# Performance work log

Hardware: AMD Instinct MI355X
Metric: run time of the kernel (lower is better)

## Reference

```python
import jax, jax.numpy as jnp
import numpy as np

N = 50000      # nodes
E = 800000     # edges (avg degree 16)
H = 128        # hidden_dim
F_IN = 128     # node_in_dim
EPS = 1e-8     # torch cosine_similarity eps
ALPHA = 0.3


def _xavier(k, shape):
    fan_out, fan_in = shape
    lim = float(np.sqrt(6.0 / (fan_in + fan_out)))
    return jax.random.uniform(k, shape, minval=-lim, maxval=lim, dtype=jnp.float32)


PARAM_SHAPES = [
    ("w_lq", (H, 1)), ("w_lf", (H, F_IN)),
    ("wq0", (H, 1)), ("wq1", (H, H)), ("wq2", (H, H)),
    ("wx0", (H, F_IN)), ("wx1", (H, H)), ("wx2", (H, H)),
    ("wf0", (H, H)), ("wf1", (H, H)), ("wf2", (H, H)),
    ("m1_w1", (H, H)), ("m1_w2", (H, H)),
    ("m2_w1", (1, H)), ("m2_w2", (1, 1)),
]
BIAS_OF = {"w_lq": "b_lq", "w_lf": "b_lf", "wq0": "bq0", "wq1": "bq1", "wq2": "bq2",
           "wx0": "bx0", "wx1": "bx1", "wx2": "bx2", "wf0": "bf0", "wf1": "bf1",
           "wf2": "bf2", "m1_w1": "m1_b1", "m1_w2": "m1_b2", "m2_w1": "m2_b1", "m2_w2": "m2_b2"}


def setup_inputs() -> dict:
    key = jax.random.key(0)
    ks = jax.random.split(key, 3 + len(PARAM_SHAPES))
    inp = {
        "q": 42,
        "feats": jax.random.normal(ks[0], (N, F_IN), dtype=jnp.float32),
        "edge_index": jax.random.randint(ks[1], (2, E), 0, N, dtype=jnp.int64),
        "neg_edge_index": jax.random.randint(ks[2], (2, E), 0, N, dtype=jnp.int64),
    }
    for i, (name, shape) in enumerate(PARAM_SHAPES):
        inp[name] = _xavier(ks[3 + i], shape)
        inp[BIAS_OF[name]] = jnp.zeros((shape[0],), jnp.float32)
    return inp


def _forward(q, feats, edge_index, neg_edge_index,
             w_lq, b_lq, w_lf, b_lf,
             wq0, bq0, wq1, bq1, wq2, bq2,
             wx0, bx0, wx1, bx1, wx2, bx2,
             wf0, bf0, wf1, bf1, wf2, bf2,
             m1_w1, m1_b1, m1_w2, m1_b2,
             m2_w1, m2_b1, m2_w2, m2_b2):
    n = feats.shape[0]
    src, dst = edge_index[0], edge_index[1]

    # GCN symmetric normalization with self-loops (edge_weight = 1)
    deg = jax.ops.segment_sum(jnp.ones(src.shape[0], feats.dtype), dst, num_segments=n) + 1.0
    dis = deg ** -0.5
    norm_e = dis[src] * dis[dst]        # per-edge norm
    inv_deg = 1.0 / deg                 # self-loop norm d^-1/2 * d^-1/2

    def lin(x, W, b):
        return x @ W.T + b

    def gcn(x, W, b):
        xw = x @ W.T                                                      # [n,H]
        agg = jax.ops.segment_sum(xw[src] * norm_e[:, None], dst, num_segments=n)
        return agg + xw * inv_deg[:, None] + b

    querys = jnp.zeros((n, 1), feats.dtype).at[q, 0].set(1.0)
    querys_ = lin(querys, w_lq, b_lq)
    feats_ = lin(feats, w_lf, b_lf)

    # layer 0
    hq = jax.nn.relu(gcn(querys, wq0, bq0))
    h = jax.nn.relu(gcn(feats, wx0, bx0))
    hf = jax.nn.relu(hq + h + gcn(querys_ + feats_, wf0, bf0))
    # middle layer (num_layers - 2 == 1 iteration, eval mode: dropout identity)
    hq = jax.nn.relu(gcn(hq, wq1, bq1))
    h = jax.nn.relu(gcn(h, wx1, bx1))
    hf = jax.nn.relu(hq + h + gcn(hf, wf1, bf1))
    # final layer (no relu)
    hq = gcn(hq, wq2, bq2)
    h = gcn(h, wx2, bx2)
    hf = hq + h + gcn(hf, wf2, bf2)

    x = lin(jax.nn.relu(lin(hf, m1_w1, m1_b1)), m1_w2, m1_b2)  # mlp1

    # ---- decode (attack_type != 'proposed') ----
    q_emb = x[q]
    qn = jnp.maximum(jnp.linalg.norm(q_emb), EPS)

    def cos_q(v):  # cosine similarity of rows of v with q_emb (torch eps semantics)
        vn = jnp.maximum(jnp.linalg.norm(v, axis=-1), EPS)
        return (v @ q_emb) / (vn * qn)

    # reconstruct loss: BCE-with-logits on cosine edge scores
    pos_s = cos_q((x[src] + x[dst]) * 0.5)
    neg_s = cos_q((x[neg_edge_index[0]] + x[neg_edge_index[1]]) * 0.5)
    loss_recon = jnp.mean(jax.nn.softplus(-pos_s)) + jnp.mean(jax.nn.softplus(neg_s))

    sim_xq = cos_q(x)                                            # [n]
    sim_xx = lin(jax.nn.relu(lin(x, m2_w1, m2_b1)), m2_w2, m2_b2)[:, 0]  # mlp2
    sim = ((1.0 - ALPHA) * sim_xq + ALPHA * sim_xx) * 2.0
    return jax.nn.sigmoid(sim), loss_recon


def reference(q, feats, edge_index, neg_edge_index,
              w_lq, b_lq, w_lf, b_lf,
              wq0, bq0, wq1, bq1, wq2, bq2,
              wx0, bx0, wx1, bx1, wx2, bx2,
              wf0, bf0, wf1, bf1, wf2, bf2,
              m1_w1, m1_b1, m1_w2, m1_b2,
              m2_w1, m2_b1, m2_w2, m2_b2):
    return _forward(q, feats, edge_index, neg_edge_index,
                    w_lq, b_lq, w_lf, b_lf,
                    wq0, bq0, wq1, bq1, wq2, bq2,
                    wx0, bx0, wx1, bx1, wx2, bx2,
                    wf0, bf0, wf1, bf1, wf2, bf2,
                    m1_w1, m1_b1, m1_w2, m1_b2,
                    m2_w1, m2_b1, m2_w2, m2_b2)
```

## Files before the change

### kernel.cpp

```cpp
#include <hip/hip_runtime.h>
#include <math.h>

#define N_NODES 50000
#define N_EDGES 800000
#define EPSV 1e-8f
#define ALPHA 0.3f

typedef __attribute__((ext_vector_type(8))) unsigned short ushort8;
typedef __attribute__((ext_vector_type(8))) short short8;
typedef __attribute__((ext_vector_type(4))) float floatx4;
typedef _Float16 half2v __attribute__((ext_vector_type(2)));

__device__ inline float b2f(unsigned short u) {
    union { unsigned i; float f; } c; c.i = ((unsigned)u) << 16; return c.f;
}
__device__ inline unsigned short f2b(float f) {
    union { float f; unsigned i; } c; c.f = f;
    return (unsigned short)((c.i + 0x7FFFu + ((c.i >> 16) & 1u)) >> 16);
}
__device__ inline unsigned short f2h(float f) {
    union { _Float16 h; unsigned short u; } c; c.h = (_Float16)f; return c.u;
}


__global__ __launch_bounds__(256) void k_count(const int* __restrict__ ei,
                                               int* __restrict__ cnt) {
    int e = blockIdx.x * 256 + threadIdx.x;
    if (e < N_EDGES) atomicAdd(&cnt[ei[N_EDGES + e]], 1);
}

__global__ __launch_bounds__(256) void k_invdis(const int* __restrict__ cnt,
                                                float* __restrict__ dis,
                                                float* __restrict__ inv) {
    int i = blockIdx.x * 256 + threadIdx.x;
    if (i < N_NODES) {
        float d = (float)cnt[i] + 1.0f;
        dis[i] = 1.0f / sqrtf(d);
        inv[i] = 1.0f / d;
    }
}

__global__ __launch_bounds__(256) void k_scan_partial(const int* __restrict__ cnt,
                                                      int* __restrict__ partial) {
    int b = blockIdx.x, t = threadIdx.x;
    int base = b * 1024 + t * 4;
    int s = 0;
#pragma unroll
    for (int j = 0; j < 4; ++j) {
        int idx = base + j;
        if (idx < N_NODES) s += cnt[idx];
    }
#pragma unroll
    for (int m = 1; m < 64; m <<= 1) s += __shfl_xor(s, m, 64);
    __shared__ int sh[4];
    if ((t & 63) == 0) sh[t >> 6] = s;
    __syncthreads();
    if (t == 0) partial[b] = sh[0] + sh[1] + sh[2] + sh[3];
}

__global__ void k_scan_mid(int* __restrict__ partial, int* __restrict__ rowptr) {
    int l = threadIdx.x;
    const int NP = (N_NODES + 1023) / 1024;
    int v = (l < NP) ? partial[l] : 0;
    int vin = v;
#pragma unroll
    for (int off = 1; off < 64; off <<= 1) {
        int u = __shfl_up(v, off, 64);
        if (l >= off) v += u;
    }
    if (l < NP) partial[l] = v - vin;
    if (l == NP - 1) rowptr[N_NODES] = v;
}

__global__ __launch_bounds__(256) void k_scan_final(const int* __restrict__ cnt,
                                                    const int* __restrict__ partial,
                                                    int* __restrict__ rowptr) {
    int b = blockIdx.x, t = threadIdx.x;
    int base = b * 1024 + t * 4;
    int c[4];
    int s = 0;
#pragma unroll
    for (int j = 0; j < 4; ++j) {
        int idx = base + j;
        c[j] = (idx < N_NODES) ? cnt[idx] : 0;
        s += c[j];
    }
    __shared__ int sh[256];
    sh[t] = s;
    __syncthreads();
    for (int off = 1; off < 256; off <<= 1) {
        int v = 0;
        if (t >= off) v = sh[t - off];
        __syncthreads();
        sh[t] += v;
        __syncthreads();
    }
    int texcl = sh[t] - s;
    int pre = partial[b] + texcl;
#pragma unroll
    for (int j = 0; j < 4; ++j) {
        int idx = base + j;
        if (idx < N_NODES) rowptr[idx] = pre;
        pre += c[j];
    }
}

__global__ __launch_bounds__(256) void k_fill(const int* __restrict__ ei,
                                              const int* __restrict__ rowptr,
                                              int* __restrict__ cursor,
                                              int* __restrict__ col) {
    int e = blockIdx.x * 256 + threadIdx.x;
    if (e < N_EDGES) {
        int d = ei[N_EDGES + e];
        int pos = rowptr[d] + atomicAdd(&cursor[d], 1);
        col[pos] = ei[e];
    }
}

__global__ __launch_bounds__(256) void k_t(const int* __restrict__ ei,
                                           const int* __restrict__ qp,
                                           const float* __restrict__ dis,
                                           const float* __restrict__ inv,
                                           float* __restrict__ t) {
    int e = blockIdx.x * 256 + threadIdx.x;
    int q = *qp;
    if (e == 0) atomicAdd(&t[q], inv[q]);
    if (e < N_EDGES && ei[e] == q) {
        int d = ei[N_EDGES + e];
        atomicAdd(&t[d], dis[q] * dis[d]);
    }
}

__global__ __launch_bounds__(256) void k_cast(const float* __restrict__ in,
                                              unsigned short* __restrict__ out, int n8) {
    int id = blockIdx.x * 256 + threadIdx.x;
    if (id >= n8) return;
    const float4 a = *(const float4*)(in + id * 8);
    const float4 b = *(const float4*)(in + id * 8 + 4);
    ushort8 o;
    o[0] = f2b(a.x); o[1] = f2b(a.y); o[2] = f2b(a.z); o[3] = f2b(a.w);
    o[4] = f2b(b.x); o[5] = f2b(b.y); o[6] = f2b(b.z); o[7] = f2b(b.w);
    *(ushort8*)(out + id * 8) = o;
}

struct WPack { const float* w[11]; };
__global__ __launch_bounds__(256) void k_castw(WPack wp, unsigned short* __restrict__ out) {
    int m = blockIdx.y;
    int id = blockIdx.x * 256 + threadIdx.x;
    const float* src = wp.w[m] + id * 8;
    float4 a = *(const float4*)src;
    float4 b = *(const float4*)(src + 4);
    ushort8 o;
    o[0] = f2b(a.x); o[1] = f2b(a.y); o[2] = f2b(a.z); o[3] = f2b(a.w);
    o[4] = f2b(b.x); o[5] = f2b(b.y); o[6] = f2b(b.z); o[7] = f2b(b.w);
    *(ushort8*)(out + m * 16384 + id * 8) = o;
}


template <int RELU, int NADD, int HASB2, int WOUT>
__global__ __launch_bounds__(256) void k_gemm(
    const unsigned short* __restrict__ A, int As,
    const unsigned short* __restrict__ Wb,
    const float* __restrict__ bias, const float* __restrict__ bias2,
    const unsigned short* __restrict__ add1, int a1s,
    const unsigned short* __restrict__ add2, int a2s,
    unsigned short* __restrict__ outh, int ohs,
    float* __restrict__ outf, int ofs, int nrows) {
    __shared__ unsigned short Al[128 * 128];
    __shared__ unsigned short Wl[128 * 128];
    const int tid = threadIdx.x;
    const int row0 = blockIdx.x * 128;
    const int wv = tid >> 6;
    const int t4 = tid >> 4, c16 = tid & 15;

#pragma unroll
    for (int it = 0; it < 8; ++it) {
        int r = it * 16 + t4;
        int gr = row0 + r; if (gr > nrows - 1) gr = nrows - 1;
        int sw = (c16 * 16) ^ ((r & 7) << 4);
        const char* srcA = (const char*)(A + (size_t)gr * As) + sw;
        __builtin_amdgcn_global_load_lds(
            (const __attribute__((address_space(1))) void*)srcA,
            (__attribute__((address_space(3))) void*)(Al + it * 2048 + wv * 512),
            16, 0, 0);
        const char* srcW = (const char*)(Wb + r * 128) + sw;
        __builtin_amdgcn_global_load_lds(
            (const __attribute__((address_space(1))) void*)srcW,
            (__attribute__((address_space(3))) void*)(Wl + it * 2048 + wv * 512),
            16, 0, 0);
    }
    __syncthreads();

    const int l = tid & 63;
    const int lr = l & 15, lg = l >> 4;
    const int sx = (lr & 7) << 4;

    floatx4 acc[8][2];
#pragma unroll
    for (int i = 0; i < 8; ++i)
#pragma unroll
        for (int j = 0; j < 2; ++j) acc[i][j] = (floatx4){0.f, 0.f, 0.f, 0.f};

#pragma unroll
    for (int ks = 0; ks < 4; ++ks) {
        int ko = (ks * 64 + lg * 16) ^ sx;
        short8 bfr[2];
#pragma unroll
        for (int ct = 0; ct < 2; ++ct) {
            int c = wv * 32 + ct * 16 + lr;
            bfr[ct] = *(const short8*)((char*)Wl + c * 256 + ko);
        }
#pragma unroll
        for (int rt = 0; rt < 8; ++rt) {
            int r = rt * 16 + lr;
            short8 af = *(const short8*)((char*)Al + r * 256 + ko);
            acc[rt][0] = __builtin_amdgcn_mfma_f32_16x16x32_bf16(af, bfr[0], acc[rt][0], 0, 0, 0);
            acc[rt][1] = __builtin_amdgcn_mfma_f32_16x16x32_bf16(af, bfr[1], acc[rt][1], 0, 0, 0);
        }
    }

#pragma unroll
    for (int ct = 0; ct < 2; ++ct) {
        int colc = wv * 32 + ct * 16 + lr;
        float bv = bias[colc];
        if (HASB2) bv += bias2[colc];
#pragma unroll
        for (int rt = 0; rt < 8; ++rt) {
            int rbase = row0 + rt * 16 + lg * 4;
#pragma unroll
            for (int reg = 0; reg < 4; ++reg) {
                int r = rbase + reg;
                if (r >= nrows) continue;
                float v = acc[rt][ct][reg] + bv;
                if (NADD >= 1) v += b2f(add1[(size_t)r * a1s + colc]);
                if (NADD >= 2) v += b2f(add2[(size_t)r * a2s + colc]);
                if (RELU) v = fmaxf(v, 0.f);
                if (WOUT) {
                    outh[(size_t)r * ohs + colc] = f2h(v);
                    outf[(size_t)r * ofs + colc] = v;
                } else {
                    outh[(size_t)r * ohs + colc] = f2b(v);
                }
            }
        }
    }
}


__global__ __launch_bounds__(256) void k_agg(
    const int* __restrict__ rowptr, const int* __restrict__ col,
    const float* __restrict__ dis, const float* __restrict__ inv,
    const unsigned short* __restrict__ in, int ins,
    unsigned short* __restrict__ out, int outs, int outcb) {
    int i = blockIdx.x * 4 + (threadIdx.x >> 6);
    int cb = blockIdx.y * 128;
    int l = threadIdx.x & 63;
    int g = l >> 4, li = l & 15;
    int r0 = rowptr[i], r1 = rowptr[i + 1];
    float acc[8] = {0.f, 0.f, 0.f, 0.f, 0.f, 0.f, 0.f, 0.f};
    for (int base = r0; base < r1; base += 4) {
        int e = base + g;
        float w = 0.f;
        int s = i;
        if (e < r1) { s = col[e]; w = dis[s]; }
        ushort8 v = *(const ushort8*)(in + (size_t)s * ins + cb + li * 8);
#pragma unroll
        for (int j = 0; j < 8; ++j) acc[j] = fmaf(w, b2f(v[j]), acc[j]);
    }
#pragma unroll
    for (int j = 0; j < 8; ++j) {
        acc[j] += __shfl_xor(acc[j], 16, 64);
        acc[j] += __shfl_xor(acc[j], 32, 64);
    }
    if (g == 0) {
        ushort8 sv = *(const ushort8*)(in + (size_t)i * ins + cb + li * 8);
        float di = dis[i], iv = inv[i];
        ushort8 o;
#pragma unroll
        for (int j = 0; j < 8; ++j) o[j] = f2b(fmaf(di, acc[j], iv * b2f(sv[j])));
        *(ushort8*)(out + (size_t)i * outs + outcb + cb + li * 8) = o;
    }
}

__global__ __launch_bounds__(256) void k_hq0(const float* __restrict__ t,
                                             const float* __restrict__ wq0,
                                             const float* __restrict__ bq0,
                                             unsigned short* __restrict__ B1h) {
    int gidx = blockIdx.x * 256 + threadIdx.x;
    int i = gidx >> 7, j = gidx & 127;
    B1h[(size_t)i * 384 + j] = f2b(fmaxf(fmaf(t[i], wq0[j], bq0[j]), 0.f));
}

__global__ void k_addwlq(const int* __restrict__ qp, const float* __restrict__ w_lq,
                         unsigned short* __restrict__ z0h) {
    int j = threadIdx.x;
    int q = *qp;
    z0h[(size_t)q * 128 + j] = f2b(b2f(z0h[(size_t)q * 128 + j]) + w_lq[j]);
}


__global__ void k_qemb(const int* __restrict__ qp, const float* __restrict__ xf,
                       float* __restrict__ qe) {
    int j = threadIdx.x;
    int q = *qp;
    float v = xf[(size_t)q * 128 + j];
    qe[j] = v;
    float s = v * v;
#pragma unroll
    for (int m = 1; m < 64; m <<= 1) s += __shfl_xor(s, m, 64);
    __shared__ float sh[2];
    if ((j & 63) == 0) sh[j >> 6] = s;
    __syncthreads();
    if (j == 0) qe[128] = fmaxf(sqrtf(sh[0] + sh[1]), EPSV);
}

__global__ __launch_bounds__(256) void k_node(const float* __restrict__ xf,
                                              const float* __restrict__ qe,
                                              const float* __restrict__ m2w1,
                                              const float* __restrict__ m2b1,
                                              const float* __restrict__ m2w2,
                                              const float* __restrict__ m2b2,
                                              float* __restrict__ out,
                                              float* __restrict__ a,
                                              float* __restrict__ n2) {
    int node = blockIdx.x * 4 + (threadIdx.x >> 6);
    int lane = threadIdx.x & 63;
    const float2 xv = *(const float2*)(xf + (size_t)node * 128 + 2 * lane);
    const float2 qv = *(const float2*)(qe + 2 * lane);
    const float2 wv = *(const float2*)(m2w1 + 2 * lane);
    float dq = xv.x * qv.x + xv.y * qv.y;
    float dx = xv.x * xv.x + xv.y * xv.y;
    float dw = xv.x * wv.x + xv.y * wv.y;
#pragma unroll
    for (int m = 1; m < 64; m <<= 1) {
        dq += __shfl_xor(dq, m, 64);
        dx += __shfl_xor(dx, m, 64);
        dw += __shfl_xor(dw, m, 64);
    }
    if (lane == 0) {
        float qn = qe[128];
        float vn = fmaxf(sqrtf(dx), EPSV);
        float simq = dq / (vn * qn);
        float l1 = dw + m2b1[0];
        float s2 = fmaxf(l1, 0.f) * m2w2[0] + m2b2[0];
        float sim = ((1.f - ALPHA) * simq + ALPHA * s2) * 2.f;
        out[node] = 1.f / (1.f + expf(-sim));
        a[node] = dq;
        n2[node] = dx;
    }
}

__global__ __launch_bounds__(256) void k_loss(const int* __restrict__ ei,
                                              const int* __restrict__ nei,
                                              const unsigned short* __restrict__ xh,
                                              const float* __restrict__ a,
                                              const float* __restrict__ n2,
                                              const float* __restrict__ qe,
                                              float* __restrict__ lossout) {
    int l = threadIdx.x & 63, wvi = threadIdx.x >> 6;
    int g = l >> 4, li = l & 15;
    float qn = qe[128];
    float local = 0.f;
    const int tot = 2 * N_EDGES;
    const int stride = gridDim.x * 16;
    for (int e = blockIdx.x * 16 + wvi * 4 + g; e < tot; e += stride) {
        const int* Ep = (e < N_EDGES) ? ei : nei;
        int eo = (e < N_EDGES) ? e : e - N_EDGES;
        int s = Ep[eo], d = Ep[eo + N_EDGES];
        union { ushort8 u; half2v h[4]; } va, vb;
        va.u = *(const ushort8*)(xh + (size_t)s * 128 + li * 8);
        vb.u = *(const ushort8*)(xh + (size_t)d * 128 + li * 8);
        float dsd = 0.f;
#pragma unroll
        for (int j = 0; j < 4; ++j)
            dsd = __builtin_amdgcn_fdot2(va.h[j], vb.h[j], dsd, false);
        dsd += __shfl_xor(dsd, 1, 64);
        dsd += __shfl_xor(dsd, 2, 64);
        dsd += __shfl_xor(dsd, 4, 64);
        dsd += __shfl_xor(dsd, 8, 64);
        if (li == 0) {
            float nv = 0.25f * (n2[s] + n2[d] + 2.f * dsd);
            float vn = fmaxf(sqrtf(fmaxf(nv, 0.f)), EPSV);
            float num = 0.5f * (a[s] + a[d]);
            float cs = num / (vn * qn);
            float sg = (e < N_EDGES) ? -cs : cs;
            local += log1pf(expf(sg));
        }
    }
    local += __shfl_xor(local, 16, 64);
    local += __shfl_xor(local, 32, 64);
    __shared__ float sh[4];
    if (l == 0) sh[wvi] = local;
    __syncthreads();
    if (threadIdx.x == 0)
        atomicAdd(lossout, (sh[0] + sh[1] + sh[2] + sh[3]) * (1.f / N_EDGES));
}


extern "C" void kernel_launch(void* const* d_in, const int* in_sizes, int n_in,
                              void* d_out, int out_size, void* d_ws, size_t ws_size,
                              hipStream_t stream) {
    const int* qp = (const int*)d_in[0];
    const float* feats = (const float*)d_in[1];
    const int* ei = (const int*)d_in[2];
    const int* nei = (const int*)d_in[3];
    const float *w_lq = (const float*)d_in[4], *b_lq = (const float*)d_in[5];
    const float *w_lf = (const float*)d_in[6], *b_lf = (const float*)d_in[7];
    const float *wq0 = (const float*)d_in[8], *bq0 = (const float*)d_in[9];
    const float *wq1 = (const float*)d_in[10], *bq1 = (const float*)d_in[11];
    const float *wq2 = (const float*)d_in[12], *bq2 = (const float*)d_in[13];
    const float *wx0 = (const float*)d_in[14], *bx0 = (const float*)d_in[15];
    const float *wx1 = (const float*)d_in[16], *bx1 = (const float*)d_in[17];
    const float *wx2 = (const float*)d_in[18], *bx2 = (const float*)d_in[19];
    const float *wf0 = (const float*)d_in[20], *bf0 = (const float*)d_in[21];
    const float *wf1 = (const float*)d_in[22], *bf1 = (const float*)d_in[23];
    const float *wf2 = (const float*)d_in[24], *bf2 = (const float*)d_in[25];
    const float *m1w1 = (const float*)d_in[26], *m1b1 = (const float*)d_in[27];
    const float *m1w2 = (const float*)d_in[28], *m1b2 = (const float*)d_in[29];
    const float *m2w1 = (const float*)d_in[30], *m2b1 = (const float*)d_in[31];
    const float *m2w2 = (const float*)d_in[32], *m2b2 = (const float*)d_in[33];
    float* out = (float*)d_out;

    char* p = (char*)d_ws;
    auto alloc = [&](size_t b) -> char* {
        char* r = p;
        p += (b + 255) & ~(size_t)255;
        return r;
    };
    float* dis = (float*)alloc(N_NODES * 4);
    float* inv = (float*)alloc(N_NODES * 4);
    float* t = (float*)alloc(N_NODES * 4);
    float* qe = (float*)alloc(129 * 4);
    float* a = (float*)alloc(N_NODES * 4);
    float* n2 = (float*)alloc(N_NODES * 4);
    int* cnt = (int*)alloc(N_NODES * 4);
    int* cursor = (int*)alloc(N_NODES * 4);
    int* rowptr = (int*)alloc((N_NODES + 1) * 4);
    int* partial = (int*)alloc(64 * 4);
    int* col = (int*)alloc(N_EDGES * 4);
    unsigned short* Wb = (unsigned short*)alloc((size_t)11 * 16384 * 2);
    unsigned short* featsh = (unsigned short*)alloc((size_t)N_NODES * 128 * 2);
    unsigned short* z0h = (unsigned short*)alloc((size_t)N_NODES * 128 * 2);
    unsigned short* B1h = (unsigned short*)alloc((size_t)N_NODES * 384 * 2);
    unsigned short* B2h = (unsigned short*)alloc((size_t)N_NODES * 384 * 2);
    unsigned short* xh = (unsigned short*)alloc((size_t)N_NODES * 128 * 2);
    float* xf = (float*)alloc((size_t)N_NODES * 128 * 4);

    const int EB = (N_EDGES + 255) / 256;
    const int NB = (N_NODES + 255) / 256;
    const int NP = (N_NODES + 1023) / 1024;
    const int GB = (N_NODES + 127) / 128;

    hipMemsetAsync(cnt, 0, N_NODES * 4, stream);
    hipMemsetAsync(cursor, 0, N_NODES * 4, stream);
    hipMemsetAsync(t, 0, N_NODES * 4, stream);
    hipMemsetAsync(out + N_NODES, 0, 4, stream);

    k_count<<<EB, 256, 0, stream>>>(ei, cnt);
    k_invdis<<<NB, 256, 0, stream>>>(cnt, dis, inv);
    k_scan_partial<<<NP, 256, 0, stream>>>(cnt, partial);
    k_scan_mid<<<1, 64, 0, stream>>>(partial, rowptr);
    k_scan_final<<<NP, 256, 0, stream>>>(cnt, partial, rowptr);
    k_fill<<<EB, 256, 0, stream>>>(ei, rowptr, cursor, col);
    k_t<<<EB, 256, 0, stream>>>(ei, qp, dis, inv, t);
    k_cast<<<(N_NODES * 128 / 8 + 255) / 256, 256, 0, stream>>>(feats, featsh,
                                                                N_NODES * 128 / 8);
    WPack wp{{w_lf, wx0, wf0, wq1, wx1, wf1, wq2, wx2, wf2, m1w1, m1w2}};
    k_castw<<<dim3(8, 11), 256, 0, stream>>>(wp, Wb);

    k_gemm<0, 0, 1, 0><<<GB, 256, 0, stream>>>(featsh, 128, Wb + 0 * 16384, b_lf, b_lq,
                                               nullptr, 0, nullptr, 0,
                                               z0h, 128, nullptr, 0, N_NODES);
    k_addwlq<<<1, 128, 0, stream>>>(qp, w_lq, z0h);

    k_hq0<<<(N_NODES * 128) / 256, 256, 0, stream>>>(t, wq0, bq0, B1h);
    k_agg<<<dim3(N_NODES / 4, 1), 256, 0, stream>>>(rowptr, col, dis, inv, featsh, 128,
                                                    B2h, 384, 128);
    k_agg<<<dim3(N_NODES / 4, 1), 256, 0, stream>>>(rowptr, col, dis, inv, z0h, 128,
                                                    B2h, 384, 256);
    k_gemm<1, 0, 0, 0><<<GB, 256, 0, stream>>>(B2h + 128, 384, Wb + 1 * 16384, bx0, nullptr,
                                               nullptr, 0, nullptr, 0,
                                               B1h + 128, 384, nullptr, 0, N_NODES);
    k_gemm<1, 2, 0, 0><<<GB, 256, 0, stream>>>(B2h + 256, 384, Wb + 2 * 16384, bf0, nullptr,
                                               B1h + 0, 384, B1h + 128, 384,
                                               B1h + 256, 384, nullptr, 0, N_NODES);

    k_agg<<<dim3(N_NODES / 4, 3), 256, 0, stream>>>(rowptr, col, dis, inv, B1h, 384,
                                                    B2h, 384, 0);
    k_gemm<1, 0, 0, 0><<<GB, 256, 0, stream>>>(B2h + 0, 384, Wb + 3 * 16384, bq1, nullptr,
                                               nullptr, 0, nullptr, 0,
                                               B1h + 0, 384, nullptr, 0, N_NODES);
    k_gemm<1, 0, 0, 0><<<GB, 256, 0, stream>>>(B2h + 128, 384, Wb + 4 * 16384, bx1, nullptr,
                                               nullptr, 0, nullptr, 0,
                                               B1h + 128, 384, nullptr, 0, N_NODES);
    k_gemm<1, 2, 0, 0><<<GB, 256, 0, stream>>>(B2h + 256, 384, Wb + 5 * 16384, bf1, nullptr,
                                               B1h + 0, 384, B1h + 128, 384,
                                               B1h + 256, 384, nullptr, 0, N_NODES);

    k_agg<<<dim3(N_NODES / 4, 3), 256, 0, stream>>>(rowptr, col, dis, inv, B1h, 384,
                                                    B2h, 384, 0);
    k_gemm<0, 0, 0, 0><<<GB, 256, 0, stream>>>(B2h + 0, 384, Wb + 6 * 16384, bq2, nullptr,
                                               nullptr, 0, nullptr, 0,
                                               B1h + 0, 384, nullptr, 0, N_NODES);
    k_gemm<0, 0, 0, 0><<<GB, 256, 0, stream>>>(B2h + 128, 384, Wb + 7 * 16384, bx2, nullptr,
                                               nullptr, 0, nullptr, 0,
                                               B1h + 128, 384, nullptr, 0, N_NODES);
    k_gemm<0, 2, 0, 0><<<GB, 256, 0, stream>>>(B2h + 256, 384, Wb + 8 * 16384, bf2, nullptr,
                                               B1h + 0, 384, B1h + 128, 384,
                                               B1h + 256, 384, nullptr, 0, N_NODES);

    k_gemm<1, 0, 0, 0><<<GB, 256, 0, stream>>>(B1h + 256, 384, Wb + 9 * 16384, m1b1, nullptr,
                                               nullptr, 0, nullptr, 0,
                                               B2h + 0, 384, nullptr, 0, N_NODES);
    k_gemm<0, 0, 0, 1><<<GB, 256, 0, stream>>>(B2h + 0, 384, Wb + 10 * 16384, m1b2, nullptr,
                                               nullptr, 0, nullptr, 0,
                                               xh, 128, xf, 128, N_NODES);

    k_qemb<<<1, 128, 0, stream>>>(qp, xf, qe);
    k_node<<<N_NODES / 4, 256, 0, stream>>>(xf, qe, m2w1, m2b1, m2w2, m2b2, out, a, n2);
    k_loss<<<4096, 256, 0, stream>>>(ei, nei, xh, a, n2, qe, out + N_NODES);
}
```

Measured before the change: 737.4 us.

## Switch intermediates to fp16, fuse multi-branch aggregation, use MFMA for edge dots

All intermediate activations and weights move from bf16 to fp16, and the GEMMs now use the f16 MFMA. The aggregation kernel handles two or three feature branches per launch and accumulates with packed half2 FMAs instead of fp32. The loss kernel computes the edge dot products with 16x16 MFMA tiles plus a bpermute instead of fdot2 and shuffle reductions. Accumulating in fp16 halves ALU and register cost but risks precision loss or overflow on high-degree nodes.

```diff
diff --git a/kernel.cpp b/kernel.cpp
--- a/kernel.cpp
+++ b/kernel.cpp
@@ -7,19 +7,15 @@
 #define ALPHA 0.3f
 
 typedef __attribute__((ext_vector_type(8))) unsigned short ushort8;
-typedef __attribute__((ext_vector_type(8))) short short8;
 typedef __attribute__((ext_vector_type(4))) float floatx4;
+typedef _Float16 half8 __attribute__((ext_vector_type(8)));
 typedef _Float16 half2v __attribute__((ext_vector_type(2)));
 
-__device__ inline float b2f(unsigned short u) {
-    union { unsigned i; float f; } c; c.i = ((unsigned)u) << 16; return c.f;
-}
-__device__ inline unsigned short f2b(float f) {
-    union { float f; unsigned i; } c; c.f = f;
-    return (unsigned short)((c.i + 0x7FFFu + ((c.i >> 16) & 1u)) >> 16);
-}
 __device__ inline unsigned short f2h(float f) {
     union { _Float16 h; unsigned short u; } c; c.h = (_Float16)f; return c.u;
+}
+__device__ inline float h2f(unsigned short u) {
+    union { unsigned short u; _Float16 h; } c; c.u = u; return (float)c.h;
 }
 
 
@@ -138,8 +134,8 @@
     const float4 a = *(const float4*)(in + id * 8);
     const float4 b = *(const float4*)(in + id * 8 + 4);
     ushort8 o;
-    o[0] = f2b(a.x); o[1] = f2b(a.y); o[2] = f2b(a.z); o[3] = f2b(a.w);
-    o[4] = f2b(b.x); o[5] = f2b(b.y); o[6] = f2b(b.z); o[7] = f2b(b.w);
+    o[0] = f2h(a.x); o[1] = f2h(a.y); o[2] = f2h(a.z); o[3] = f2h(a.w);
+    o[4] = f2h(b.x); o[5] = f2h(b.y); o[6] = f2h(b.z); o[7] = f2h(b.w);
     *(ushort8*)(out + id * 8) = o;
 }
 
@@ -151,8 +147,8 @@
     float4 a = *(const float4*)src;
     float4 b = *(const float4*)(src + 4);
     ushort8 o;
-    o[0] = f2b(a.x); o[1] = f2b(a.y); o[2] = f2b(a.z); o[3] = f2b(a.w);
-    o[4] = f2b(b.x); o[5] = f2b(b.y); o[6] = f2b(b.z); o[7] = f2b(b.w);
+    o[0] = f2h(a.x); o[1] = f2h(a.y); o[2] = f2h(a.z); o[3] = f2h(a.w);
+    o[4] = f2h(b.x); o[5] = f2h(b.y); o[6] = f2h(b.z); o[7] = f2h(b.w);
     *(ushort8*)(out + m * 16384 + id * 8) = o;
 }
 
@@ -204,18 +200,18 @@
 #pragma unroll
     for (int ks = 0; ks < 4; ++ks) {
         int ko = (ks * 64 + lg * 16) ^ sx;
-        short8 bfr[2];
+        half8 bfr[2];
 #pragma unroll
         for (int ct = 0; ct < 2; ++ct) {
             int c = wv * 32 + ct * 16 + lr;
-            bfr[ct] = *(const short8*)((char*)Wl + c * 256 + ko);
+            bfr[ct] = *(const half8*)((char*)Wl + c * 256 + ko);
         }
 #pragma unroll
         for (int rt = 0; rt < 8; ++rt) {
             int r = rt * 16 + lr;
-            short8 af = *(const short8*)((char*)Al + r * 256 + ko);
-            acc[rt][0] = __builtin_amdgcn_mfma_f32_16x16x32_bf16(af, bfr[0], acc[rt][0], 0, 0, 0);
-            acc[rt][1] = __builtin_amdgcn_mfma_f32_16x16x32_bf16(af, bfr[1], acc[rt][1], 0, 0, 0);
+            half8 af = *(const half8*)((char*)Al + r * 256 + ko);
+            acc[rt][0] = __builtin_amdgcn_mfma_f32_16x16x32_f16(af, bfr[0], acc[rt][0], 0, 0, 0);
+            acc[rt][1] = __builtin_amdgcn_mfma_f32_16x16x32_f16(af, bfr[1], acc[rt][1], 0, 0, 0);
         }
     }
 
@@ -232,53 +228,89 @@
                 int r = rbase + reg;
                 if (r >= nrows) continue;
                 float v = acc[rt][ct][reg] + bv;
-                if (NADD >= 1) v += b2f(add1[(size_t)r * a1s + colc]);
-                if (NADD >= 2) v += b2f(add2[(size_t)r * a2s + colc]);
+                if (NADD >= 1) v += h2f(add1[(size_t)r * a1s + colc]);
+                if (NADD >= 2) v += h2f(add2[(size_t)r * a2s + colc]);
                 if (RELU) v = fmaxf(v, 0.f);
-                if (WOUT) {
-                    outh[(size_t)r * ohs + colc] = f2h(v);
-                    outf[(size_t)r * ofs + colc] = v;
-                } else {
-                    outh[(size_t)r * ohs + colc] = f2b(v);
-                }
+                outh[(size_t)r * ohs + colc] = f2h(v);
+                if (WOUT) outf[(size_t)r * ofs + colc] = v;
             }
         }
     }
 }
 
 
+template <int NUM>
 __global__ __launch_bounds__(256) void k_agg(
     const int* __restrict__ rowptr, const int* __restrict__ col,
     const float* __restrict__ dis, const float* __restrict__ inv,
-    const unsigned short* __restrict__ in, int ins,
-    unsigned short* __restrict__ out, int outs, int outcb) {
+    const unsigned short* __restrict__ in0, int s0,
+    const unsigned short* __restrict__ in1, int s1,
+    const unsigned short* __restrict__ in2, int s2,
+    unsigned short* __restrict__ out, int o0, int o1, int o2) {
     int i = blockIdx.x * 4 + (threadIdx.x >> 6);
-    int cb = blockIdx.y * 128;
     int l = threadIdx.x & 63;
     int g = l >> 4, li = l & 15;
     int r0 = rowptr[i], r1 = rowptr[i + 1];
-    float acc[8] = {0.f, 0.f, 0.f, 0.f, 0.f, 0.f, 0.f, 0.f};
+
+    half2v acc[NUM][4];
+#pragma unroll
+    for (int b = 0; b < NUM; ++b)
+#pragma unroll
+        for (int j = 0; j < 4; ++j) acc[b][j] = (half2v){(_Float16)0, (_Float16)0};
+
+    union U8 { ushort8 u; half2v h[4]; };
     for (int base = r0; base < r1; base += 4) {
         int e = base + g;
         float w = 0.f;
         int s = i;
         if (e < r1) { s = col[e]; w = dis[s]; }
-        ushort8 v = *(const ushort8*)(in + (size_t)s * ins + cb + li * 8);
-#pragma unroll
-        for (int j = 0; j < 8; ++j) acc[j] = fmaf(w, b2f(v[j]), acc[j]);
-    }
-#pragma unroll
-    for (int j = 0; j < 8; ++j) {
-        acc[j] += __shfl_xor(acc[j], 16, 64);
-        acc[j] += __shfl_xor(acc[j], 32, 64);
-    }
+        _Float16 wh = (_Float16)w;
+        half2v w2 = {wh, wh};
+        U8 v;
+        v.u = *(const ushort8*)(in0 + (size_t)s * s0 + li * 8);
+#pragma unroll
+        for (int j = 0; j < 4; ++j) acc[0][j] += v.h[j] * w2;
+        if (NUM > 1) {
+            v.u = *(const ushort8*)(in1 + (size_t)s * s1 + li * 8);
+#pragma unroll
+            for (int j = 0; j < 4; ++j) acc[1][j] += v.h[j] * w2;
+        }
+        if (NUM > 2) {
+            v.u = *(const ushort8*)(in2 + (size_t)s * s2 + li * 8);
+#pragma unroll
+            for (int j = 0; j < 4; ++j) acc[2][j] += v.h[j] * w2;
+        }
+    }
+    union U2 { half2v h; int i; };
+#pragma unroll
+    for (int b = 0; b < NUM; ++b)
+#pragma unroll
+        for (int j = 0; j < 4; ++j) {
+            U2 c, o;
+            c.h = acc[b][j];
+            o.i = __shfl_xor(c.i, 16, 64); c.h += o.h;
+            o.i = __shfl_xor(c.i, 32, 64); c.h += o.h;
+            acc[b][j] = c.h;
+        }
     if (g == 0) {
-        ushort8 sv = *(const ushort8*)(in + (size_t)i * ins + cb + li * 8);
         float di = dis[i], iv = inv[i];
-        ushort8 o;
-#pragma unroll
-        for (int j = 0; j < 8; ++j) o[j] = f2b(fmaf(di, acc[j], iv * b2f(sv[j])));
-        *(ushort8*)(out + (size_t)i * outs + outcb + cb + li * 8) = o;
+        const unsigned short* ins[3] = {in0, in1, in2};
+        const int ss[3] = {s0, s1, s2};
+        const int oo[3] = {o0, o1, o2};
+#pragma unroll
+        for (int b = 0; b < NUM; ++b) {
+            U8 sv;
+            sv.u = *(const ushort8*)(ins[b] + (size_t)i * ss[b] + li * 8);
+            ushort8 o;
+#pragma unroll
+            for (int j = 0; j < 4; ++j) {
+                float a0 = fmaf(di, (float)acc[b][j][0], iv * (float)sv.h[j][0]);
+                float a1 = fmaf(di, (float)acc[b][j][1], iv * (float)sv.h[j][1]);
+                o[2 * j] = f2h(a0);
+                o[2 * j + 1] = f2h(a1);
+            }
+            *(ushort8*)(out + (size_t)i * 384 + oo[b] + li * 8) = o;
+        }
     }
 }
 
@@ -288,14 +320,14 @@
                                              unsigned short* __restrict__ B1h) {
     int gidx = blockIdx.x * 256 + threadIdx.x;
     int i = gidx >> 7, j = gidx & 127;
-    B1h[(size_t)i * 384 + j] = f2b(fmaxf(fmaf(t[i], wq0[j], bq0[j]), 0.f));
+    B1h[(size_t)i * 384 + j] = f2h(fmaxf(fmaf(t[i], wq0[j], bq0[j]), 0.f));
 }
 
 __global__ void k_addwlq(const int* __restrict__ qp, const float* __restrict__ w_lq,
                          unsigned short* __restrict__ z0h) {
     int j = threadIdx.x;
     int q = *qp;
-    z0h[(size_t)q * 128 + j] = f2b(b2f(z0h[(size_t)q * 128 + j]) + w_lq[j]);
+    z0h[(size_t)q * 128 + j] = f2h(h2f(z0h[(size_t)q * 128 + j]) + w_lq[j]);
 }
 
 
@@ -358,37 +390,52 @@
                                               const float* __restrict__ qe,
                                               float* __restrict__ lossout) {
     int l = threadIdx.x & 63, wvi = threadIdx.x >> 6;
-    int g = l >> 4, li = l & 15;
+    int i16 = l & 15;
+    int kb = l >> 4;
+    int gw = blockIdx.x * 4 + wvi;
+    const int NW16 = gridDim.x * 4 * 16;
     float qn = qe[128];
     float local = 0.f;
-    const int tot = 2 * N_EDGES;
-    const int stride = gridDim.x * 16;
-    for (int e = blockIdx.x * 16 + wvi * 4 + g; e < tot; e += stride) {
-        const int* Ep = (e < N_EDGES) ? ei : nei;
-        int eo = (e < N_EDGES) ? e : e - N_EDGES;
-        int s = Ep[eo], d = Ep[eo + N_EDGES];
-        union { ushort8 u; half2v h[4]; } va, vb;
-        va.u = *(const ushort8*)(xh + (size_t)s * 128 + li * 8);
-        vb.u = *(const ushort8*)(xh + (size_t)d * 128 + li * 8);
-        float dsd = 0.f;
-#pragma unroll
-        for (int j = 0; j < 4; ++j)
-            dsd = __builtin_amdgcn_fdot2(va.h[j], vb.h[j], dsd, false);
-        dsd += __shfl_xor(dsd, 1, 64);
-        dsd += __shfl_xor(dsd, 2, 64);
-        dsd += __shfl_xor(dsd, 4, 64);
-        dsd += __shfl_xor(dsd, 8, 64);
-        if (li == 0) {
+
+    for (int base = gw * 16; base < 2 * N_EDGES; base += NW16) {
+        const int neg = (base >= N_EDGES);
+        const int* Ep = neg ? nei : ei;
+        int eo = neg ? base - N_EDGES : base;
+        int s = Ep[eo + i16];
+        int d = Ep[eo + i16 + N_EDGES];
+        const unsigned short* ps = xh + (size_t)s * 128 + kb * 8;
+        const unsigned short* pd = xh + (size_t)d * 128 + kb * 8;
+        half8 af[4], bf[4];
+#pragma unroll
+        for (int ks = 0; ks < 4; ++ks) {
+            af[ks] = *(const half8*)(ps + ks * 32);
+            bf[ks] = *(const half8*)(pd + ks * 32);
+        }
+        floatx4 acc = (floatx4){0.f, 0.f, 0.f, 0.f};
+#pragma unroll
+        for (int ks = 0; ks < 4; ++ks)
+            acc = __builtin_amdgcn_mfma_f32_16x16x32_f16(af[ks], bf[ks], acc, 0, 0, 0);
+        int r = l & 3;
+        float v = acc[0];
+        v = (r == 1) ? acc[1] : v;
+        v = (r == 2) ? acc[2] : v;
+        v = (r == 3) ? acc[3] : v;
+        int srcl = ((i16 >> 2) << 4) + i16;
+        float dsd = __int_as_float(
+            __builtin_amdgcn_ds_bpermute(srcl << 2, __float_as_int(v)));
+        if (l < 16) {
             float nv = 0.25f * (n2[s] + n2[d] + 2.f * dsd);
             float vn = fmaxf(sqrtf(fmaxf(nv, 0.f)), EPSV);
             float num = 0.5f * (a[s] + a[d]);
             float cs = num / (vn * qn);
-            float sg = (e < N_EDGES) ? -cs : cs;
+            float sg = neg ? cs : -cs;
             local += log1pf(expf(sg));
         }
     }
-    local += __shfl_xor(local, 16, 64);
-    local += __shfl_xor(local, 32, 64);
+    local += __shfl_xor(local, 1, 64);
+    local += __shfl_xor(local, 2, 64);
+    local += __shfl_xor(local, 4, 64);
+    local += __shfl_xor(local, 8, 64);
     __shared__ float sh[4];
     if (l == 0) sh[wvi] = local;
     __syncthreads();
@@ -474,10 +521,9 @@
     k_addwlq<<<1, 128, 0, stream>>>(qp, w_lq, z0h);
 
     k_hq0<<<(N_NODES * 128) / 256, 256, 0, stream>>>(t, wq0, bq0, B1h);
-    k_agg<<<dim3(N_NODES / 4, 1), 256, 0, stream>>>(rowptr, col, dis, inv, featsh, 128,
-                                                    B2h, 384, 128);
-    k_agg<<<dim3(N_NODES / 4, 1), 256, 0, stream>>>(rowptr, col, dis, inv, z0h, 128,
-                                                    B2h, 384, 256);
+    k_agg<2><<<N_NODES / 4, 256, 0, stream>>>(rowptr, col, dis, inv,
+                                              featsh, 128, z0h, 128, nullptr, 0,
+                                              B2h, 128, 256, 0);
     k_gemm<1, 0, 0, 0><<<GB, 256, 0, stream>>>(B2h + 128, 384, Wb + 1 * 16384, bx0, nullptr,
                                                nullptr, 0, nullptr, 0,
                                                B1h + 128, 384, nullptr, 0, N_NODES);
@@ -485,8 +531,9 @@
                                                B1h + 0, 384, B1h + 128, 384,
                                                B1h + 256, 384, nullptr, 0, N_NODES);
 
-    k_agg<<<dim3(N_NODES / 4, 3), 256, 0, stream>>>(rowptr, col, dis, inv, B1h, 384,
-                                                    B2h, 384, 0);
+    k_agg<3><<<N_NODES / 4, 256, 0, stream>>>(rowptr, col, dis, inv,
+                                              B1h, 384, B1h + 128, 384, B1h + 256, 384,
+                                              B2h, 0, 128, 256);
     k_gemm<1, 0, 0, 0><<<GB, 256, 0, stream>>>(B2h + 0, 384, Wb + 3 * 16384, bq1, nullptr,
                                                nullptr, 0, nullptr, 0,
                                                B1h + 0, 384, nullptr, 0, N_NODES);
@@ -497,8 +544,9 @@
                                                B1h + 0, 384, B1h + 128, 384,
                                                B1h + 256, 384, nullptr, 0, N_NODES);
 
-    k_agg<<<dim3(N_NODES / 4, 3), 256, 0, stream>>>(rowptr, col, dis, inv, B1h, 384,
-                                                    B2h, 384, 0);
+    k_agg<3><<<N_NODES / 4, 256, 0, stream>>>(rowptr, col, dis, inv,
+                                              B1h, 384, B1h + 128, 384, B1h + 256, 384,
+                                              B2h, 0, 128, 256);
     k_gemm<0, 0, 0, 0><<<GB, 256, 0, stream>>>(B2h + 0, 384, Wb + 6 * 16384, bq2, nullptr,
                                                nullptr, 0, nullptr, 0,
                                                B1h + 0, 384, nullptr, 0, N_NODES);
```

Measured after the change: 686.3 us. -6.9%, faster.
